# Kernel optimization log

Measured on AMD Instinct MI355X. Metric: run time of the kernel, lower is better.

The kernel has to match this reference:

```python
import jax, jax.numpy as jnp
import numpy as np
from jax.ops import segment_sum

NUM_GRAPHS = 64


def _leaky_relu(x):
    return jnp.where(x >= 0, x, 0.01 * x)


def setup_inputs() -> dict:
    key = jax.random.key(0)
    ks = jax.random.split(key, 8)
    N, E, D = 100000, 1600000, 128
    x = jax.random.normal(ks[0], (N, D), dtype=jnp.float32)
    edge_index = jax.random.randint(ks[1], (2, E), 0, N, dtype=jnp.int64)
    batch = jnp.sort(jax.random.randint(ks[2], (N,), 0, NUM_GRAPHS, dtype=jnp.int64))
    s = 1.0 / np.sqrt(D)
    W1 = jax.random.normal(ks[3], (D, D), dtype=jnp.float32) * s
    b1 = jnp.zeros((D,), dtype=jnp.float32)
    W2 = jax.random.normal(ks[4], (D, D), dtype=jnp.float32) * s
    b2 = jnp.zeros((D,), dtype=jnp.float32)
    fcW = jax.random.normal(ks[5], (D, 1), dtype=jnp.float32) * s
    fcb = jnp.zeros((1,), dtype=jnp.float32)
    return {"x": x, "edge_index": edge_index, "batch": batch,
            "W1": W1, "b1": b1, "W2": W2, "b2": b2, "fcW": fcW, "fcb": fcb}


def reference(x, edge_index, batch, W1, b1, W2, b2, fcW, fcb):
    N = x.shape[0]
    # GCNConv: add self-loops, symmetric normalization D^-1/2 A D^-1/2
    loop = jnp.arange(N, dtype=edge_index.dtype)
    row = jnp.concatenate([edge_index[0], loop])  # source j
    col = jnp.concatenate([edge_index[1], loop])  # target i
    deg = segment_sum(jnp.ones_like(col, dtype=x.dtype), col, num_segments=N)
    dis = jax.lax.rsqrt(deg)  # deg >= 1 due to self-loops
    norm = dis[row] * dis[col]  # [E+N]

    def conv(h, W, b):
        h = h @ W                               # [N, D'] linear transform
        msg = h[row] * norm[:, None]            # gather + scale
        agg = segment_sum(msg, col, num_segments=N)  # scatter-add
        return agg + b

    h = _leaky_relu(conv(x, W1, b1))
    h = _leaky_relu(conv(h, W2, b2))

    # global_mean_pool over batch ids
    sums = segment_sum(h, batch, num_segments=NUM_GRAPHS)
    cnts = segment_sum(jnp.ones((N,), dtype=h.dtype), batch, num_segments=NUM_GRAPHS)
    pooled = sums / jnp.maximum(cnts, 1.0)[:, None]
    return pooled @ fcW + fcb  # [NUM_GRAPHS, 1]
```

## Files before the change

kernel.cpp:

```cpp
#include <hip/hip_runtime.h>
#include <hip/hip_bf16.h>
#include <math.h>

#define D 128
#define NUM_GRAPHS 64
#define CHUNK 8192
#define BUCK_SH 8
#define BUCK_N 256
#define BCAP 8192

typedef __bf16 bf16x8 __attribute__((ext_vector_type(8)));
typedef __bf16 bf16x2 __attribute__((ext_vector_type(2)));
typedef float f32x4 __attribute__((ext_vector_type(4)));
typedef float f32x2 __attribute__((ext_vector_type(2)));

__device__ inline unsigned char f32_to_fp8(float x) {
    int pk = __builtin_amdgcn_cvt_pk_fp8_f32(x, x, 0, false);
    return (unsigned char)(pk & 0xff);
}
__device__ inline f32x2 fp8x2_to_f32(unsigned short us) {
    return __builtin_amdgcn_cvt_pk_f32_fp8((unsigned int)us, false);
}

__global__ void k_prepW(const float* __restrict__ Wa, const float* __restrict__ Wb,
                        __bf16* __restrict__ WfA, __bf16* __restrict__ WfB,
                        float* __restrict__ pooled,
                        int* __restrict__ gcur,
                        const int* __restrict__ batch, int* __restrict__ gstart, int N) {
    int gid = blockIdx.x * 256 + threadIdx.x;
    if (gid < NUM_GRAPHS * D) pooled[gid] = 0.f;
    if (gid < 512) gcur[gid] = 0;
    if (gid >= 16384 && gid <= 16384 + NUM_GRAPHS) {
        int g = gid - 16384;
        int lo = 0, hi = N;
        while (lo < hi) { int mid = (lo + hi) >> 1; if (batch[mid] < g) lo = mid + 1; else hi = mid; }
        gstart[g] = lo;
    }
    if (gid >= 32768) return;
    const float* W = (gid < 16384) ? Wa : Wb;
    __bf16* Wf = (gid < 16384) ? WfA : WfB;
    int idx = gid & 16383;
    int j = idx & 7, lane = (idx >> 3) & 63, kc = (idx >> 9) & 3, ft = idx >> 11;
    int k = kc * 32 + (lane >> 4) * 8 + j;
    int f = ft * 16 + (lane & 15);
    Wf[idx] = (__bf16)W[k * D + f];
}

template <typename T>
__device__ __forceinline__ void gemm_body(int bid, int tid, const T* __restrict__ X,
                                          const __bf16* __restrict__ Wfrag,
                                          unsigned char* __restrict__ Y8, int N) {
    int w = tid >> 6, lane = tid & 63;
    int quad = lane >> 4, m = lane & 15;
    int nodeA = bid * 64 + w * 16 + m;
    if (nodeA >= N) nodeA = N - 1;

    bf16x8 a[4];
#pragma unroll
    for (int kc = 0; kc < 4; kc++) {
        int kb = kc * 32 + quad * 8;
        if constexpr (sizeof(T) == 4) {
            f32x4 x0 = *(const f32x4*)(X + (size_t)nodeA * D + kb);
            f32x4 x1 = *(const f32x4*)(X + (size_t)nodeA * D + kb + 4);
#pragma unroll
            for (int j = 0; j < 4; j++) { a[kc][j] = (__bf16)x0[j]; a[kc][4 + j] = (__bf16)x1[j]; }
        } else {
            a[kc] = *(const bf16x8*)(X + (size_t)nodeA * D + kb);
        }
    }

    f32x4 d[8];
#pragma unroll
    for (int ft = 0; ft < 8; ft++) {
        d[ft] = (f32x4){0.f, 0.f, 0.f, 0.f};
#pragma unroll
        for (int kc = 0; kc < 4; kc++) {
            bf16x8 b = *(const bf16x8*)(Wfrag + (((ft << 2) | kc) * 64 + lane) * 8);
            d[ft] = __builtin_amdgcn_mfma_f32_16x16x32_bf16(a[kc], b, d[ft], 0, 0, 0);
        }
    }

#pragma unroll
    for (int r = 0; r < 4; r++) {
        int node = bid * 64 + w * 16 + quad * 4 + r;
        if (node < N) {
#pragma unroll
            for (int ft = 0; ft < 8; ft++)
                Y8[(size_t)node * D + ft * 16 + m] = f32_to_fp8(d[ft][r]);
        }
    }
}

__launch_bounds__(256)
__global__ void k_bin_gemm(const int* __restrict__ ei, int* __restrict__ gcur,
                           int* __restrict__ bbuf, int nbuck, int E, int nchunk,
                           const float* __restrict__ X, const __bf16* __restrict__ Wfrag,
                           unsigned char* __restrict__ Y8, int N) {
    __shared__ int h[512];
    __shared__ int base[512];

    if (blockIdx.x >= nchunk) {
        gemm_body<float>(blockIdx.x - nchunk, threadIdx.x, X, Wfrag, Y8, N);
        return;
    }

    int tid = threadIdx.x;
    for (int b = tid; b < nbuck; b += 256) h[b] = 0;
    __syncthreads();
    int lo = blockIdx.x * CHUNK;
    if (lo + CHUNK <= E) {
        const int4* c4 = (const int4*)(ei + E + lo);
#pragma unroll 2
        for (int i = tid; i < CHUNK / 4; i += 256) {
            int4 c = c4[i];
            atomicAdd(&h[c.x >> BUCK_SH], 1);
            atomicAdd(&h[c.y >> BUCK_SH], 1);
            atomicAdd(&h[c.z >> BUCK_SH], 1);
            atomicAdd(&h[c.w >> BUCK_SH], 1);
        }
    } else {
        for (int i = tid; i < CHUNK; i += 256) {
            int e = lo + i;
            if (e < E) atomicAdd(&h[ei[E + e] >> BUCK_SH], 1);
        }
    }
    __syncthreads();
    for (int b = tid; b < nbuck; b += 256) {
        base[b] = atomicAdd(&gcur[b], h[b]);
        h[b] = 0;
    }
    __syncthreads();
    if (lo + CHUNK <= E) {
        const int4* r4 = (const int4*)(ei + lo);
        const int4* c4 = (const int4*)(ei + E + lo);
#pragma unroll 2
        for (int i = tid; i < CHUNK / 4; i += 256) {
            int4 r = r4[i];
            int4 c = c4[i];
            int rr[4] = {r.x, r.y, r.z, r.w};
            int cc[4] = {c.x, c.y, c.z, c.w};
#pragma unroll
            for (int u = 0; u < 4; u++) {
                int b = cc[u] >> BUCK_SH;
                int pos = base[b] + atomicAdd(&h[b], 1);
                if (pos < BCAP) bbuf[(size_t)b * BCAP + pos] = rr[u] | ((cc[u] & (BUCK_N - 1)) << 17);
            }
        }
    } else {
        for (int i = tid; i < CHUNK; i += 256) {
            int e = lo + i;
            if (e < E) {
                int r = ei[e], c = ei[E + e];
                int b = c >> BUCK_SH;
                int pos = base[b] + atomicAdd(&h[b], 1);
                if (pos < BCAP) bbuf[(size_t)b * BCAP + pos] = r | ((c & (BUCK_N - 1)) << 17);
            }
        }
    }
}

__global__ void k_place(const int* __restrict__ bbuf, const int* __restrict__ gcur,
                        int* __restrict__ esrc,
                        int* __restrict__ cnt, int* __restrict__ offs,
                        float* __restrict__ dis, int N) {
    __shared__ int h[256];
    __shared__ int sc[256];
    __shared__ int cur[256];
    int b = blockIdx.x, tid = threadIdx.x;
    int start = b * BCAP;
    int count = gcur[b]; if (count > BCAP) count = BCAP;
    int end = start + count;
    h[tid] = 0;
    __syncthreads();
    for (int i = start + tid; i < end; i += 256) atomicAdd(&h[(bbuf[i] >> 17) & 255], 1);
    __syncthreads();
    int local = h[tid];
    sc[tid] = local;
    __syncthreads();
    for (int off = 1; off < 256; off <<= 1) {
        int xv = (tid >= off) ? sc[tid - off] : 0;
        __syncthreads();
        sc[tid] += xv;
        __syncthreads();
    }
    int excl = sc[tid] - local;
    cur[tid] = start + excl;
    int c = b * 256 + tid;
    if (c < N) {
        cnt[c]  = local;
        offs[c] = start + excl;
        dis[c]  = rsqrtf(1.0f + (float)local);
    }
    __syncthreads();
    for (int i = start + tid; i < end; i += 256) {
        int p = bbuf[i];
        int pos = atomicAdd(&cur[(p >> 17) & 255], 1);
        esrc[pos] = p & 0x1FFFF;
    }
}

__launch_bounds__(256)
__global__ void k_gemm2(const __bf16* __restrict__ X, const __bf16* __restrict__ Wfrag,
                        unsigned char* __restrict__ Y8, int N) {
    gemm_body<__bf16>(blockIdx.x, threadIdx.x, X, Wfrag, Y8, N);
}

template <int POOL>
__launch_bounds__(256)
__global__ void k_agg(const unsigned char* __restrict__ Hs8, __bf16* __restrict__ O,
                      const int* __restrict__ offs, const int* __restrict__ cnt,
                      const float* __restrict__ dis, const int* __restrict__ esrc,
                      const float* __restrict__ bias,
                      const int* __restrict__ batch, float* __restrict__ pooled, int N) {
    int wave = (blockIdx.x * 256 + threadIdx.x) >> 6;
    int lane = threadIdx.x & 63;
    int node0 = wave * 8;
    float b0 = bias[lane * 2], b1 = bias[lane * 2 + 1];

    float s0 = 0.f, s1 = 0.f;
    int curg = -1;

    for (int nn = 0; nn < 8; nn++) {
        int node = node0 + nn;
        if (node >= N) break;
        int start = offs[node];
        int len = cnt[node];
        float di = dis[node];
        f32x2 h = fp8x2_to_f32(*(const unsigned short*)(Hs8 + (size_t)node * D + lane * 2));
        float acc0 = h[0] * di;
        float acc1 = h[1] * di;

        for (int k0 = 0; k0 < len; k0 += 64) {
            int mm = len - k0; if (mm > 64) mm = 64;
            int ep = esrc[start + k0 + (lane < mm ? lane : 0)];
            float dvl = dis[ep];
            int j = 0;
            for (; j + 16 <= mm; j += 16) {
                int s[16]; float dv[16]; unsigned short hv[16];
#pragma unroll
                for (int u = 0; u < 16; u++) { s[u] = __shfl(ep, j + u); dv[u] = __shfl(dvl, j + u); }
#pragma unroll
                for (int u = 0; u < 16; u++) hv[u] = *(const unsigned short*)(Hs8 + (size_t)s[u] * D + lane * 2);
#pragma unroll
                for (int u = 0; u < 16; u++) { f32x2 f = fp8x2_to_f32(hv[u]); acc0 += f[0] * dv[u]; acc1 += f[1] * dv[u]; }
            }
            for (; j + 4 <= mm; j += 4) {
                int s[4]; float dv[4]; unsigned short hv[4];
#pragma unroll
                for (int u = 0; u < 4; u++) { s[u] = __shfl(ep, j + u); dv[u] = __shfl(dvl, j + u); }
#pragma unroll
                for (int u = 0; u < 4; u++) hv[u] = *(const unsigned short*)(Hs8 + (size_t)s[u] * D + lane * 2);
#pragma unroll
                for (int u = 0; u < 4; u++) { f32x2 f = fp8x2_to_f32(hv[u]); acc0 += f[0] * dv[u]; acc1 += f[1] * dv[u]; }
            }
            for (; j < mm; j++) {
                int s = __shfl(ep, j);
                float dv = __shfl(dvl, j);
                f32x2 f = fp8x2_to_f32(*(const unsigned short*)(Hs8 + (size_t)s * D + lane * 2));
                acc0 += f[0] * dv; acc1 += f[1] * dv;
            }
        }

        acc0 = acc0 * di + b0;
        acc1 = acc1 * di + b1;
        acc0 = acc0 >= 0.f ? acc0 : 0.01f * acc0;
        acc1 = acc1 >= 0.f ? acc1 : 0.01f * acc1;

        if constexpr (POOL) {
            int g = batch[node];
            if (g != curg) {
                if (curg >= 0) {
                    atomicAdd(&pooled[curg * D + lane * 2],     s0);
                    atomicAdd(&pooled[curg * D + lane * 2 + 1], s1);
                }
                curg = g; s0 = 0.f; s1 = 0.f;
            }
            s0 += acc0; s1 += acc1;
        } else {
            bf16x2 o; o[0] = (__bf16)acc0; o[1] = (__bf16)acc1;
            *(bf16x2*)(O + (size_t)node * D + lane * 2) = o;
        }
    }

    if constexpr (POOL) {
        if (curg >= 0) {
            atomicAdd(&pooled[curg * D + lane * 2],     s0);
            atomicAdd(&pooled[curg * D + lane * 2 + 1], s1);
        }
    }
}

__launch_bounds__(64)
__global__ void k_fc(const float* __restrict__ pooled, const int* __restrict__ gstart,
                     const float* __restrict__ fcW, const float* __restrict__ fcb,
                     float* __restrict__ out) {
    int t = threadIdx.x;
    float s = 0.f;
#pragma unroll 8
    for (int k = 0; k < D; k += 4) {
        f32x4 pv = *(const f32x4*)(pooled + t * D + k);
        f32x4 wv = *(const f32x4*)(fcW + k);
        s += pv[0] * wv[0] + pv[1] * wv[1] + pv[2] * wv[2] + pv[3] * wv[3];
    }
    float c = (float)(gstart[t + 1] - gstart[t]);
    out[t] = s / fmaxf(c, 1.0f) + fcb[0];
}

extern "C" void kernel_launch(void* const* d_in, const int* in_sizes, int n_in,
                              void* d_out, int out_size, void* d_ws, size_t ws_size,
                              hipStream_t stream) {
    const float* x    = (const float*)d_in[0];
    const int*   ei   = (const int*)d_in[1];
    const int*   batch= (const int*)d_in[2];
    const float* W1   = (const float*)d_in[3];
    const float* b1   = (const float*)d_in[4];
    const float* W2   = (const float*)d_in[5];
    const float* b2   = (const float*)d_in[6];
    const float* fcW  = (const float*)d_in[7];
    const float* fcb  = (const float*)d_in[8];
    float* out = (float*)d_out;

    int N = in_sizes[0] / D;
    int E = in_sizes[1] / 2;

    int NBUCK  = (N + BUCK_N - 1) >> BUCK_SH;
    int NCHUNK = (E + CHUNK - 1) / CHUNK;

    char* p = (char*)d_ws;
    auto alloc = [&](size_t bytes) { char* r = p; p += (bytes + 255) & ~(size_t)255; return r; };
    int*    cnt    = (int*)   alloc((size_t)N * 4);
    int*    offs   = (int*)   alloc((size_t)N * 4);
    float*  dis    = (float*) alloc((size_t)N * 4);
    int*    gcur   = (int*)   alloc(512 * 4);
    int*    bbuf   = (int*)   alloc((size_t)NBUCK * BCAP * 4);
    int*    esrc   = (int*)   alloc((size_t)NBUCK * BCAP * 4);
    unsigned char* bufA8 = (unsigned char*)alloc((size_t)N * D);
    __bf16* bufB   = (__bf16*)alloc((size_t)N * D * 2);
    __bf16* Wf1    = (__bf16*)alloc((size_t)D * D * 2);
    __bf16* Wf2    = (__bf16*)alloc((size_t)D * D * 2);
    float*  pooled = (float*) alloc((size_t)NUM_GRAPHS * D * 4);
    int*    gstart = (int*)   alloc((NUM_GRAPHS + 1) * 4);

    int gblocks = (N + 63) / 64;
    int ablocks = (N + 31) / 32;

    k_prepW<<<129, 256, 0, stream>>>(W1, W2, Wf1, Wf2, pooled, gcur, batch, gstart, N);

    k_bin_gemm<<<NCHUNK + gblocks, 256, 0, stream>>>(ei, gcur, bbuf, NBUCK, E, NCHUNK,
                                                     x, Wf1, bufA8, N);
    k_place<<<NBUCK, 256, 0, stream>>>(bbuf, gcur, esrc, cnt, offs, dis, N);

    k_agg<0><<<ablocks, 256, 0, stream>>>(bufA8, bufB, offs, cnt, dis, esrc, b1,
                                          batch, pooled, N);
    k_gemm2<<<gblocks, 256, 0, stream>>>(bufB, Wf2, bufA8, N);
    k_agg<1><<<ablocks, 256, 0, stream>>>(bufA8, nullptr, offs, cnt, dis, esrc, b2,
                                          batch, pooled, N);
    k_fc<<<1, 64, 0, stream>>>(pooled, gstart, fcW, fcb, out);
}
```

Measured before the change: 318.2 us.

## Fold source-side degree normalization into GEMM epilogue to drop per-edge scaling

Adds a global-atomic degree histogram to the prep kernel so the first GEMM can scale each output row by its rsqrt(degree) before fp8 quantization; the second GEMM scales by the precomputed dis. The aggregation kernels then sum pre-scaled neighbor rows without gathering dis[src] or shuffling per-edge weights. This removes one random gather and two shuffles per edge, at the cost of an extra memset, 1.6M global atomics in a new histogram pass, and quantizing pre-scaled values to fp8.

```diff
diff --git a/kernel.cpp b/kernel.cpp
--- a/kernel.cpp
+++ b/kernel.cpp
@@ -8,6 +8,8 @@
 #define BUCK_SH 8
 #define BUCK_N 256
 #define BCAP 8192
+#define PREP_BLOCKS 129
+#define HIST_BLOCKS 400
 
 typedef __bf16 bf16x8 __attribute__((ext_vector_type(8)));
 typedef __bf16 bf16x2 __attribute__((ext_vector_type(2)));
@@ -26,7 +28,24 @@
                         __bf16* __restrict__ WfA, __bf16* __restrict__ WfB,
                         float* __restrict__ pooled,
                         int* __restrict__ gcur,
-                        const int* __restrict__ batch, int* __restrict__ gstart, int N) {
+                        const int* __restrict__ batch, int* __restrict__ gstart, int N,
+                        const int* __restrict__ ei, int E, int* __restrict__ deg) {
+    if (blockIdx.x >= PREP_BLOCKS) {
+        int tid = (blockIdx.x - PREP_BLOCKS) * 256 + threadIdx.x;
+        int nthreads = HIST_BLOCKS * 256;
+        const int* col = ei + E;
+        int n4 = E >> 2;
+        const int4* c4 = (const int4*)col;
+        for (int i = tid; i < n4; i += nthreads) {
+            int4 c = c4[i];
+            atomicAdd(&deg[c.x], 1);
+            atomicAdd(&deg[c.y], 1);
+            atomicAdd(&deg[c.z], 1);
+            atomicAdd(&deg[c.w], 1);
+        }
+        if (tid < (E & 3)) atomicAdd(&deg[col[(n4 << 2) + tid]], 1);
+        return;
+    }
     int gid = blockIdx.x * 256 + threadIdx.x;
     if (gid < NUM_GRAPHS * D) pooled[gid] = 0.f;
     if (gid < 512) gcur[gid] = 0;
@@ -46,9 +65,11 @@
     Wf[idx] = (__bf16)W[k * D + f];
 }
 
-template <typename T>
+template <typename T, int SMODE>
 __device__ __forceinline__ void gemm_body(int bid, int tid, const T* __restrict__ X,
                                           const __bf16* __restrict__ Wfrag,
+                                          const int* __restrict__ deg,
+                                          const float* __restrict__ dis,
                                           unsigned char* __restrict__ Y8, int N) {
     int w = tid >> 6, lane = tid & 63;
     int quad = lane >> 4, m = lane & 15;
@@ -80,13 +101,35 @@
         }
     }
 
+    int nb = bid * 64 + w * 16 + quad * 4;
+    float sc[4];
+    if constexpr (SMODE == 1) {
+        if (nb + 3 < N) {
+            int4 dg = *(const int4*)(deg + nb);
+            sc[0] = rsqrtf(1.f + (float)dg.x); sc[1] = rsqrtf(1.f + (float)dg.y);
+            sc[2] = rsqrtf(1.f + (float)dg.z); sc[3] = rsqrtf(1.f + (float)dg.w);
+        } else {
+#pragma unroll
+            for (int r = 0; r < 4; r++) sc[r] = (nb + r < N) ? rsqrtf(1.f + (float)deg[nb + r]) : 0.f;
+        }
+    } else {
+        if (nb + 3 < N) {
+            f32x4 dv = *(const f32x4*)(dis + nb);
+#pragma unroll
+            for (int r = 0; r < 4; r++) sc[r] = dv[r];
+        } else {
+#pragma unroll
+            for (int r = 0; r < 4; r++) sc[r] = (nb + r < N) ? dis[nb + r] : 0.f;
+        }
+    }
+
 #pragma unroll
     for (int r = 0; r < 4; r++) {
-        int node = bid * 64 + w * 16 + quad * 4 + r;
+        int node = nb + r;
         if (node < N) {
 #pragma unroll
             for (int ft = 0; ft < 8; ft++)
-                Y8[(size_t)node * D + ft * 16 + m] = f32_to_fp8(d[ft][r]);
+                Y8[(size_t)node * D + ft * 16 + m] = f32_to_fp8(d[ft][r] * sc[r]);
         }
     }
 }
@@ -95,12 +138,13 @@
 __global__ void k_bin_gemm(const int* __restrict__ ei, int* __restrict__ gcur,
                            int* __restrict__ bbuf, int nbuck, int E, int nchunk,
                            const float* __restrict__ X, const __bf16* __restrict__ Wfrag,
+                           const int* __restrict__ deg,
                            unsigned char* __restrict__ Y8, int N) {
     __shared__ int h[512];
     __shared__ int base[512];
 
     if (blockIdx.x >= nchunk) {
-        gemm_body<float>(blockIdx.x - nchunk, threadIdx.x, X, Wfrag, Y8, N);
+        gemm_body<float, 1>(blockIdx.x - nchunk, threadIdx.x, X, Wfrag, deg, nullptr, Y8, N);
         return;
     }
 
@@ -201,8 +245,9 @@
 
 __launch_bounds__(256)
 __global__ void k_gemm2(const __bf16* __restrict__ X, const __bf16* __restrict__ Wfrag,
+                        const float* __restrict__ dis,
                         unsigned char* __restrict__ Y8, int N) {
-    gemm_body<__bf16>(blockIdx.x, threadIdx.x, X, Wfrag, Y8, N);
+    gemm_body<__bf16, 2>(blockIdx.x, threadIdx.x, X, Wfrag, nullptr, dis, Y8, N);
 }
 
 template <int POOL>
@@ -227,37 +272,35 @@
         int len = cnt[node];
         float di = dis[node];
         f32x2 h = fp8x2_to_f32(*(const unsigned short*)(Hs8 + (size_t)node * D + lane * 2));
-        float acc0 = h[0] * di;
-        float acc1 = h[1] * di;
+        float acc0 = h[0];
+        float acc1 = h[1];
 
         for (int k0 = 0; k0 < len; k0 += 64) {
             int mm = len - k0; if (mm > 64) mm = 64;
             int ep = esrc[start + k0 + (lane < mm ? lane : 0)];
-            float dvl = dis[ep];
             int j = 0;
             for (; j + 16 <= mm; j += 16) {
-                int s[16]; float dv[16]; unsigned short hv[16];
-#pragma unroll
-                for (int u = 0; u < 16; u++) { s[u] = __shfl(ep, j + u); dv[u] = __shfl(dvl, j + u); }
+                int s[16]; unsigned short hv[16];
+#pragma unroll
+                for (int u = 0; u < 16; u++) s[u] = __shfl(ep, j + u);
 #pragma unroll
                 for (int u = 0; u < 16; u++) hv[u] = *(const unsigned short*)(Hs8 + (size_t)s[u] * D + lane * 2);
 #pragma unroll
-                for (int u = 0; u < 16; u++) { f32x2 f = fp8x2_to_f32(hv[u]); acc0 += f[0] * dv[u]; acc1 += f[1] * dv[u]; }
+                for (int u = 0; u < 16; u++) { f32x2 f = fp8x2_to_f32(hv[u]); acc0 += f[0]; acc1 += f[1]; }
             }
             for (; j + 4 <= mm; j += 4) {
-                int s[4]; float dv[4]; unsigned short hv[4];
-#pragma unroll
-                for (int u = 0; u < 4; u++) { s[u] = __shfl(ep, j + u); dv[u] = __shfl(dvl, j + u); }
+                int s[4]; unsigned short hv[4];
+#pragma unroll
+                for (int u = 0; u < 4; u++) s[u] = __shfl(ep, j + u);
 #pragma unroll
                 for (int u = 0; u < 4; u++) hv[u] = *(const unsigned short*)(Hs8 + (size_t)s[u] * D + lane * 2);
 #pragma unroll
-                for (int u = 0; u < 4; u++) { f32x2 f = fp8x2_to_f32(hv[u]); acc0 += f[0] * dv[u]; acc1 += f[1] * dv[u]; }
+                for (int u = 0; u < 4; u++) { f32x2 f = fp8x2_to_f32(hv[u]); acc0 += f[0]; acc1 += f[1]; }
             }
             for (; j < mm; j++) {
                 int s = __shfl(ep, j);
-                float dv = __shfl(dvl, j);
                 f32x2 f = fp8x2_to_f32(*(const unsigned short*)(Hs8 + (size_t)s * D + lane * 2));
-                acc0 += f[0] * dv; acc1 += f[1] * dv;
+                acc0 += f[0]; acc1 += f[1];
             }
         }
 
@@ -331,6 +374,7 @@
     int*    cnt    = (int*)   alloc((size_t)N * 4);
     int*    offs   = (int*)   alloc((size_t)N * 4);
     float*  dis    = (float*) alloc((size_t)N * 4);
+    int*    deg    = (int*)   alloc((size_t)N * 4);
     int*    gcur   = (int*)   alloc(512 * 4);
     int*    bbuf   = (int*)   alloc((size_t)NBUCK * BCAP * 4);
     int*    esrc   = (int*)   alloc((size_t)NBUCK * BCAP * 4);
@@ -344,15 +388,17 @@
     int gblocks = (N + 63) / 64;
     int ablocks = (N + 31) / 32;
 
-    k_prepW<<<129, 256, 0, stream>>>(W1, W2, Wf1, Wf2, pooled, gcur, batch, gstart, N);
+    hipMemsetAsync(deg, 0, (size_t)N * 4, stream);
+    k_prepW<<<PREP_BLOCKS + HIST_BLOCKS, 256, 0, stream>>>(
+        W1, W2, Wf1, Wf2, pooled, gcur, batch, gstart, N, ei, E, deg);
 
     k_bin_gemm<<<NCHUNK + gblocks, 256, 0, stream>>>(ei, gcur, bbuf, NBUCK, E, NCHUNK,
-                                                     x, Wf1, bufA8, N);
+                                                     x, Wf1, deg, bufA8, N);
     k_place<<<NBUCK, 256, 0, stream>>>(bbuf, gcur, esrc, cnt, offs, dis, N);
 
     k_agg<0><<<ablocks, 256, 0, stream>>>(bufA8, bufB, offs, cnt, dis, esrc, b1,
                                           batch, pooled, N);
-    k_gemm2<<<gblocks, 256, 0, stream>>>(bufB, Wf2, bufA8, N);
+    k_gemm2<<<gblocks, 256, 0, stream>>>(bufB, Wf2, dis, bufA8, N);
     k_agg<1><<<ablocks, 256, 0, stream>>>(bufA8, nullptr, offs, cnt, dis, esrc, b2,
                                           batch, pooled, N);
     k_fc<<<1, 64, 0, stream>>>(pooled, gstart, fcW, fcb, out);
```

Result: slower. 352.2 us (+10.7%).

## Fuse layer-1 aggregation with layer-2 GEMM, pre-scale rows, split pooling out

Applied to the files above, without the earlier changes.

Layer-1 aggregation results now stay in LDS as bf16 and feed an MFMA GEMM inside the same kernel. The output rows are pre-scaled by the source node's dis, so layer-2 aggregation no longer gathers dis per edge or multiplies by it. The mean-pool atomics move out of the aggregation kernel into a separate per-graph slice reduction kernel. This drops a bf16 intermediate round trip and per-edge work, at the cost of an extra bf16 write and read of the layer-2 output for the pool kernel.

```diff
diff --git a/kernel.cpp b/kernel.cpp
--- a/kernel.cpp
+++ b/kernel.cpp
@@ -8,6 +8,8 @@
 #define BUCK_SH 8
 #define BUCK_N 256
 #define BCAP 8192
+#define PSLICE 8
+#define HROW 136
 
 typedef __bf16 bf16x8 __attribute__((ext_vector_type(8)));
 typedef __bf16 bf16x2 __attribute__((ext_vector_type(2)));
@@ -200,64 +202,149 @@
 }
 
 __launch_bounds__(256)
-__global__ void k_gemm2(const __bf16* __restrict__ X, const __bf16* __restrict__ Wfrag,
-                        unsigned char* __restrict__ Y8, int N) {
-    gemm_body<__bf16>(blockIdx.x, threadIdx.x, X, Wfrag, Y8, N);
-}
-
-template <int POOL>
+__global__ void k_agg_gemm(const unsigned char* __restrict__ Hs8,
+                           const int* __restrict__ offs, const int* __restrict__ cnt,
+                           const float* __restrict__ dis, const int* __restrict__ esrc,
+                           const float* __restrict__ bias,
+                           const __bf16* __restrict__ Wfrag,
+                           unsigned char* __restrict__ Y8, int N) {
+    __shared__ __bf16 hl[32 * HROW];
+    int tid = threadIdx.x;
+    int w = tid >> 6, lane = tid & 63;
+    int node0 = blockIdx.x * 32 + w * 8;
+    float b0 = bias[lane * 2], b1v = bias[lane * 2 + 1];
+
+    for (int nn = 0; nn < 8; nn++) {
+        int node = node0 + nn;
+        if (node < N) {
+            int start = offs[node];
+            int len = cnt[node];
+            float di = dis[node];
+            f32x2 h = fp8x2_to_f32(*(const unsigned short*)(Hs8 + (size_t)node * D + lane * 2));
+            float acc0 = h[0] * di;
+            float acc1 = h[1] * di;
+
+            for (int k0 = 0; k0 < len; k0 += 64) {
+                int mm = len - k0; if (mm > 64) mm = 64;
+                int ep = esrc[start + k0 + (lane < mm ? lane : 0)];
+                float dvl = dis[ep];
+                int j = 0;
+                for (; j + 16 <= mm; j += 16) {
+                    int s[16]; float dv[16]; unsigned short hv[16];
+#pragma unroll
+                    for (int u = 0; u < 16; u++) { s[u] = __shfl(ep, j + u); dv[u] = __shfl(dvl, j + u); }
+#pragma unroll
+                    for (int u = 0; u < 16; u++) hv[u] = *(const unsigned short*)(Hs8 + (size_t)s[u] * D + lane * 2);
+#pragma unroll
+                    for (int u = 0; u < 16; u++) { f32x2 f = fp8x2_to_f32(hv[u]); acc0 += f[0] * dv[u]; acc1 += f[1] * dv[u]; }
+                }
+                for (; j + 4 <= mm; j += 4) {
+                    int s[4]; float dv[4]; unsigned short hv[4];
+#pragma unroll
+                    for (int u = 0; u < 4; u++) { s[u] = __shfl(ep, j + u); dv[u] = __shfl(dvl, j + u); }
+#pragma unroll
+                    for (int u = 0; u < 4; u++) hv[u] = *(const unsigned short*)(Hs8 + (size_t)s[u] * D + lane * 2);
+#pragma unroll
+                    for (int u = 0; u < 4; u++) { f32x2 f = fp8x2_to_f32(hv[u]); acc0 += f[0] * dv[u]; acc1 += f[1] * dv[u]; }
+                }
+                for (; j < mm; j++) {
+                    int s = __shfl(ep, j);
+                    float dv = __shfl(dvl, j);
+                    f32x2 f = fp8x2_to_f32(*(const unsigned short*)(Hs8 + (size_t)s * D + lane * 2));
+                    acc0 += f[0] * dv; acc1 += f[1] * dv;
+                }
+            }
+
+            acc0 = acc0 * di + b0;
+            acc1 = acc1 * di + b1v;
+            acc0 = acc0 >= 0.f ? acc0 : 0.01f * acc0;
+            acc1 = acc1 >= 0.f ? acc1 : 0.01f * acc1;
+            bf16x2 o; o[0] = (__bf16)acc0; o[1] = (__bf16)acc1;
+            *(bf16x2*)&hl[(w * 8 + nn) * HROW + lane * 2] = o;
+        } else {
+            bf16x2 z; z[0] = (__bf16)0.f; z[1] = (__bf16)0.f;
+            *(bf16x2*)&hl[(w * 8 + nn) * HROW + lane * 2] = z;
+        }
+    }
+    __syncthreads();
+
+    int quad = lane >> 4, m = lane & 15;
+    int rtile = w & 1, fthalf = w >> 1;
+    int lrow = rtile * 16 + m;
+    bf16x8 a[4];
+#pragma unroll
+    for (int kc = 0; kc < 4; kc++)
+        a[kc] = *(const bf16x8*)&hl[lrow * HROW + kc * 32 + quad * 8];
+
+    int nb = blockIdx.x * 32 + rtile * 16 + quad * 4;
+    float scv[4];
+#pragma unroll
+    for (int r = 0; r < 4; r++) scv[r] = (nb + r < N) ? dis[nb + r] : 0.f;
+
+#pragma unroll
+    for (int ft = 0; ft < 4; ft++) {
+        int gft = fthalf * 4 + ft;
+        f32x4 dacc = (f32x4){0.f, 0.f, 0.f, 0.f};
+#pragma unroll
+        for (int kc = 0; kc < 4; kc++) {
+            bf16x8 b = *(const bf16x8*)(Wfrag + (((gft << 2) | kc) * 64 + lane) * 8);
+            dacc = __builtin_amdgcn_mfma_f32_16x16x32_bf16(a[kc], b, dacc, 0, 0, 0);
+        }
+#pragma unroll
+        for (int r = 0; r < 4; r++) {
+            int node = nb + r;
+            if (node < N)
+                Y8[(size_t)node * D + gft * 16 + m] = f32_to_fp8(dacc[r] * scv[r]);
+        }
+    }
+}
+
 __launch_bounds__(256)
 __global__ void k_agg(const unsigned char* __restrict__ Hs8, __bf16* __restrict__ O,
                       const int* __restrict__ offs, const int* __restrict__ cnt,
                       const float* __restrict__ dis, const int* __restrict__ esrc,
-                      const float* __restrict__ bias,
-                      const int* __restrict__ batch, float* __restrict__ pooled, int N) {
+                      const float* __restrict__ bias, int N) {
     int wave = (blockIdx.x * 256 + threadIdx.x) >> 6;
     int lane = threadIdx.x & 63;
     int node0 = wave * 8;
     float b0 = bias[lane * 2], b1 = bias[lane * 2 + 1];
 
-    float s0 = 0.f, s1 = 0.f;
-    int curg = -1;
-
     for (int nn = 0; nn < 8; nn++) {
         int node = node0 + nn;
-        if (node >= N) break;
+        if (node >= N) return;
         int start = offs[node];
         int len = cnt[node];
         float di = dis[node];
         f32x2 h = fp8x2_to_f32(*(const unsigned short*)(Hs8 + (size_t)node * D + lane * 2));
-        float acc0 = h[0] * di;
-        float acc1 = h[1] * di;
+        float acc0 = h[0];
+        float acc1 = h[1];
 
         for (int k0 = 0; k0 < len; k0 += 64) {
             int mm = len - k0; if (mm > 64) mm = 64;
             int ep = esrc[start + k0 + (lane < mm ? lane : 0)];
-            float dvl = dis[ep];
             int j = 0;
             for (; j + 16 <= mm; j += 16) {
-                int s[16]; float dv[16]; unsigned short hv[16];
-#pragma unroll
-                for (int u = 0; u < 16; u++) { s[u] = __shfl(ep, j + u); dv[u] = __shfl(dvl, j + u); }
+                int s[16]; unsigned short hv[16];
+#pragma unroll
+                for (int u = 0; u < 16; u++) s[u] = __shfl(ep, j + u);
 #pragma unroll
                 for (int u = 0; u < 16; u++) hv[u] = *(const unsigned short*)(Hs8 + (size_t)s[u] * D + lane * 2);
 #pragma unroll
-                for (int u = 0; u < 16; u++) { f32x2 f = fp8x2_to_f32(hv[u]); acc0 += f[0] * dv[u]; acc1 += f[1] * dv[u]; }
+                for (int u = 0; u < 16; u++) { f32x2 f = fp8x2_to_f32(hv[u]); acc0 += f[0]; acc1 += f[1]; }
             }
             for (; j + 4 <= mm; j += 4) {
-                int s[4]; float dv[4]; unsigned short hv[4];
-#pragma unroll
-                for (int u = 0; u < 4; u++) { s[u] = __shfl(ep, j + u); dv[u] = __shfl(dvl, j + u); }
+                int s[4]; unsigned short hv[4];
+#pragma unroll
+                for (int u = 0; u < 4; u++) s[u] = __shfl(ep, j + u);
 #pragma unroll
                 for (int u = 0; u < 4; u++) hv[u] = *(const unsigned short*)(Hs8 + (size_t)s[u] * D + lane * 2);
 #pragma unroll
-                for (int u = 0; u < 4; u++) { f32x2 f = fp8x2_to_f32(hv[u]); acc0 += f[0] * dv[u]; acc1 += f[1] * dv[u]; }
+                for (int u = 0; u < 4; u++) { f32x2 f = fp8x2_to_f32(hv[u]); acc0 += f[0]; acc1 += f[1]; }
             }
             for (; j < mm; j++) {
                 int s = __shfl(ep, j);
-                float dv = __shfl(dvl, j);
                 f32x2 f = fp8x2_to_f32(*(const unsigned short*)(Hs8 + (size_t)s * D + lane * 2));
-                acc0 += f[0] * dv; acc1 += f[1] * dv;
+                acc0 += f[0]; acc1 += f[1];
             }
         }
 
@@ -265,28 +352,46 @@
         acc1 = acc1 * di + b1;
         acc0 = acc0 >= 0.f ? acc0 : 0.01f * acc0;
         acc1 = acc1 >= 0.f ? acc1 : 0.01f * acc1;
-
-        if constexpr (POOL) {
-            int g = batch[node];
-            if (g != curg) {
-                if (curg >= 0) {
-                    atomicAdd(&pooled[curg * D + lane * 2],     s0);
-                    atomicAdd(&pooled[curg * D + lane * 2 + 1], s1);
-                }
-                curg = g; s0 = 0.f; s1 = 0.f;
-            }
-            s0 += acc0; s1 += acc1;
-        } else {
-            bf16x2 o; o[0] = (__bf16)acc0; o[1] = (__bf16)acc1;
-            *(bf16x2*)(O + (size_t)node * D + lane * 2) = o;
-        }
-    }
-
-    if constexpr (POOL) {
-        if (curg >= 0) {
-            atomicAdd(&pooled[curg * D + lane * 2],     s0);
-            atomicAdd(&pooled[curg * D + lane * 2 + 1], s1);
-        }
+        bf16x2 o; o[0] = (__bf16)acc0; o[1] = (__bf16)acc1;
+        *(bf16x2*)(O + (size_t)node * D + lane * 2) = o;
+    }
+}
+
+__launch_bounds__(256)
+__global__ void k_pool(const __bf16* __restrict__ H, const int* __restrict__ gstart,
+                       float* __restrict__ pooled) {
+    __shared__ float sdata[256 * 9];
+    int g = blockIdx.x / PSLICE;
+    int slice = blockIdx.x - g * PSLICE;
+    int gs = gstart[g], ge = gstart[g + 1];
+    int cg = ge - gs;
+    int r0 = gs + (int)((long long)cg * slice / PSLICE);
+    int r1 = gs + (int)((long long)cg * (slice + 1) / PSLICE);
+    int t = threadIdx.x;
+    int rg = t >> 4, fb = t & 15;
+
+    float acc[8];
+#pragma unroll
+    for (int j = 0; j < 8; j++) acc[j] = 0.f;
+    for (int r = r0 + rg; r < r1; r += 16) {
+        bf16x8 v = *(const bf16x8*)(H + (size_t)r * D + fb * 8);
+#pragma unroll
+        for (int j = 0; j < 8; j++) acc[j] += (float)v[j];
+    }
+#pragma unroll
+    for (int j = 0; j < 8; j++) sdata[t * 9 + j] = acc[j];
+    __syncthreads();
+#pragma unroll
+    for (int s = 128; s >= 16; s >>= 1) {
+        if (t < s) {
+#pragma unroll
+            for (int j = 0; j < 8; j++) sdata[t * 9 + j] += sdata[(t + s) * 9 + j];
+        }
+        __syncthreads();
+    }
+    if (t < 16) {
+#pragma unroll
+        for (int j = 0; j < 8; j++) atomicAdd(&pooled[g * D + t * 8 + j], sdata[t * 9 + j]);
     }
 }
 
@@ -335,6 +440,7 @@
     int*    bbuf   = (int*)   alloc((size_t)NBUCK * BCAP * 4);
     int*    esrc   = (int*)   alloc((size_t)NBUCK * BCAP * 4);
     unsigned char* bufA8 = (unsigned char*)alloc((size_t)N * D);
+    unsigned char* bufC8 = (unsigned char*)alloc((size_t)N * D);
     __bf16* bufB   = (__bf16*)alloc((size_t)N * D * 2);
     __bf16* Wf1    = (__bf16*)alloc((size_t)D * D * 2);
     __bf16* Wf2    = (__bf16*)alloc((size_t)D * D * 2);
@@ -350,10 +456,10 @@
                                                      x, Wf1, bufA8, N);
     k_place<<<NBUCK, 256, 0, stream>>>(bbuf, gcur, esrc, cnt, offs, dis, N);
 
-    k_agg<0><<<ablocks, 256, 0, stream>>>(bufA8, bufB, offs, cnt, dis, esrc, b1,
-                                          batch, pooled, N);
-    k_gemm2<<<gblocks, 256, 0, stream>>>(bufB, Wf2, bufA8, N);
-    k_agg<1><<<ablocks, 256, 0, stream>>>(bufA8, nullptr, offs, cnt, dis, esrc, b2,
-                                          batch, pooled, N);
+    k_agg_gemm<<<ablocks, 256, 0, stream>>>(bufA8, offs, cnt, dis, esrc, b1, Wf2, bufC8, N);
+
+    k_agg<<<ablocks, 256, 0, stream>>>(bufC8, bufB, offs, cnt, dis, esrc, b2, N);
+
+    k_pool<<<NUM_GRAPHS * PSLICE, 256, 0, stream>>>(bufB, gstart, pooled);
     k_fc<<<1, 64, 0, stream>>>(pooled, gstart, fcW, fcb, out);
 }
```

After: 292.1 us. 1.09x faster.
